# Performance work log

Hardware: AMD Instinct MI355X
Metric: run time of the kernel (lower is better)

The kernel has to match this reference:

```python
import jax, jax.numpy as jnp
import numpy as np

H = 16          # num_heads
LN_EPS = 1e-5   # torch LayerNorm default


def _ln(x, g, b):
    m = jnp.mean(x, axis=-1, keepdims=True)
    v = jnp.var(x, axis=-1, keepdims=True)
    return (x - m) * jax.lax.rsqrt(v + LN_EPS) * g + b


def _cross_attn(xq, xkv, wq, wk, wv, wp, bp):
    B, N, C = xq.shape
    d = C // H
    scale = d ** -0.5
    q = (xq @ wq).reshape(B, N, H, d).transpose(0, 2, 1, 3)   # bhnd
    k = (xkv @ wk).reshape(B, N, H, d).transpose(0, 2, 1, 3)
    v = (xkv @ wv).reshape(B, N, H, d).transpose(0, 2, 1, 3)
    attn = jax.nn.softmax(jnp.einsum('bhnd,bhmd->bhnm', q, k) * scale, axis=-1)
    out = jnp.einsum('bhnm,bhmd->bhnd', attn, v).transpose(0, 2, 1, 3).reshape(B, N, C)
    return out @ wp + bp


def setup_inputs() -> dict:
    key = jax.random.key(0)
    ks = jax.random.split(key, 16)
    B, N, C, Hid = 8, 1024, 1024, 4096
    s = 0.02
    inp = {
        'x_1': jax.random.normal(ks[0], (B, N, C), jnp.float32),
        'x_2': jax.random.normal(ks[1], (B, N, C), jnp.float32),
        'x_3': jax.random.normal(ks[2], (B, N, C), jnp.float32),
        'ln11_g': jnp.ones((C,), jnp.float32), 'ln11_b': jnp.zeros((C,), jnp.float32),
        'ln12_g': jnp.ones((C,), jnp.float32), 'ln12_b': jnp.zeros((C,), jnp.float32),
        'ln21_g': jnp.ones((C,), jnp.float32), 'ln21_b': jnp.zeros((C,), jnp.float32),
        'ln23_g': jnp.ones((C,), jnp.float32), 'ln23_b': jnp.zeros((C,), jnp.float32),
        'ln2_g': jnp.ones((C,), jnp.float32), 'ln2_b': jnp.zeros((C,), jnp.float32),
        'a1_wq': s * jax.random.normal(ks[3], (C, C), jnp.float32),
        'a1_wk': s * jax.random.normal(ks[4], (C, C), jnp.float32),
        'a1_wv': s * jax.random.normal(ks[5], (C, C), jnp.float32),
        'a1_wp': s * jax.random.normal(ks[6], (C, C), jnp.float32),
        'a1_bp': jnp.zeros((C,), jnp.float32),
        'a2_wq': s * jax.random.normal(ks[7], (C, C), jnp.float32),
        'a2_wk': s * jax.random.normal(ks[8], (C, C), jnp.float32),
        'a2_wv': s * jax.random.normal(ks[9], (C, C), jnp.float32),
        'a2_wp': s * jax.random.normal(ks[10], (C, C), jnp.float32),
        'a2_bp': jnp.zeros((C,), jnp.float32),
        'fc1_w': s * jax.random.normal(ks[11], (C, Hid), jnp.float32),
        'fc1_b': jnp.zeros((Hid,), jnp.float32),
        'fc2_w': s * jax.random.normal(ks[12], (Hid, C), jnp.float32),
        'fc2_b': jnp.zeros((C,), jnp.float32),
    }
    return inp


def reference(x_1, x_2, x_3,
              ln11_g, ln11_b, ln12_g, ln12_b, ln21_g, ln21_b, ln23_g, ln23_b,
              ln2_g, ln2_b,
              a1_wq, a1_wk, a1_wv, a1_wp, a1_bp,
              a2_wq, a2_wk, a2_wv, a2_wp, a2_bp,
              fc1_w, fc1_b, fc2_w, fc2_b):
    # dual cross-attention branches + residual (drop_path/dropout are identity at p=0)
    br1 = _cross_attn(_ln(x_1, ln11_g, ln11_b), _ln(x_2, ln12_g, ln12_b),
                      a1_wq, a1_wk, a1_wv, a1_wp, a1_bp)
    br2 = _cross_attn(_ln(x_1, ln21_g, ln21_b), _ln(x_3, ln23_g, ln23_b),
                      a2_wq, a2_wk, a2_wv, a2_wp, a2_bp)
    x = x_1 + br1 + br2
    # MLP block
    h = jax.nn.gelu(_ln(x, ln2_g, ln2_b) @ fc1_w + fc1_b, approximate=False)
    x = x + (h @ fc2_w + fc2_b)
    return x
```

## Files before the change

### kernel.cpp

```cpp
#include <hip/hip_runtime.h>
#include <hip/hip_bf16.h>
#include <cstdint>

typedef unsigned short u16;
typedef __bf16 v8bf __attribute__((ext_vector_type(8)));
typedef short v4s __attribute__((ext_vector_type(4)));
typedef float v4f __attribute__((ext_vector_type(4)));

__device__ __forceinline__ u16 f2bf(float f) {
  union { float f; uint32_t u; } v; v.f = f;
  return (u16)((v.u + 0x7fffu + ((v.u >> 16) & 1u)) >> 16);
}
__device__ __forceinline__ float bf2f(u16 u) {
  union { uint32_t u; float f; } v; v.u = ((uint32_t)u) << 16; return v.f;
}

#define GLL16(gsrc, ldst) \
  __builtin_amdgcn_global_load_lds((__attribute__((address_space(1))) void*)(gsrc), \
      (__attribute__((address_space(3))) void*)(ldst), 16, 0, 0)

#define TILE_MAP(blk, bm, bn) \
  int bm = ((blk) & 7) * 8 + (((blk) >> 3) & 7); \
  int bn = (blk) >> 6;

__device__ __forceinline__ void gemm_core(
    const u16* __restrict__ A, const u16* __restrict__ Bt, int K,
    char* la, char* lb, int bm, int bn, int tid, v4f acc[4][4])
{
  int wv = tid >> 6, lane = tid & 63, quad = lane >> 4, lc = lane & 15;
  int wm = wv & 1, wn = wv >> 1;
  for (int kt = 0; kt < K; kt += 64) {
    __syncthreads();
    #pragma unroll
    for (int c0 = 0; c0 < 4; ++c0) {
      int chunk = wv*4 + c0;
      int off = chunk*1024 + lane*16;
      int row = off >> 7;
      int sc  = (off >> 4) & 7;
      int lg  = sc ^ (row & 7);
      GLL16(A  + (size_t)(bm*128 + row) * K + kt + lg*8, la + chunk*1024);
      GLL16(Bt + (size_t)(bn*128 + row) * K + kt + lg*8, lb + chunk*1024);
    }
    __syncthreads();
    #pragma unroll
    for (int kc = 0; kc < 2; ++kc) {
      v8bf af[4], bfr[4];
      #pragma unroll
      for (int r = 0; r < 4; ++r) {
        int row = wm*64 + r*16 + lc;
        int sc = (kc*4 + quad) ^ (row & 7);
        af[r] = *(const v8bf*)(la + row*128 + sc*16);
      }
      #pragma unroll
      for (int c = 0; c < 4; ++c) {
        int row = wn*64 + c*16 + lc;
        int sc = (kc*4 + quad) ^ (row & 7);
        bfr[c] = *(const v8bf*)(lb + row*128 + sc*16);
      }
      #pragma unroll
      for (int r = 0; r < 4; ++r)
        #pragma unroll
        for (int c = 0; c < 4; ++c)
          acc[r][c] = __builtin_amdgcn_mfma_f32_16x16x32_bf16(af[r], bfr[c], acc[r][c], 0, 0, 0);
    }
  }
}

struct TDesc { const float* W; u16* WT; int K, N, tstart; };
struct PrepArgs {
  TDesc d[10];
  const float* lx[4]; const float* lg[4]; const float* lb_[4]; u16* lo[4];
  int ts;
};
__global__ __launch_bounds__(256) void prep_kernel(PrepArgs P)
{
  __shared__ float sh[32*33];
  int tid = threadIdx.x;
  if ((int)blockIdx.x < P.ts) {
    int bi = blockIdx.x;
    int idx = 0;
    #pragma unroll
    for (int i = 1; i < 10; ++i) if (bi >= P.d[i].tstart) idx = i;
    const float* W = P.d[idx].W;
    u16* WT = P.d[idx].WT;
    int K = P.d[idx].K, N = P.d[idx].N;
    int loc = bi - P.d[idx].tstart;
    int tiles_n = N >> 5;
    int bn = loc % tiles_n, bk = loc / tiles_n;
    int tx = tid & 31, ty = tid >> 5;
    #pragma unroll
    for (int j = 0; j < 4; ++j)
      sh[(ty + j*8)*33 + tx] = W[(size_t)(bk*32 + ty + j*8) * N + bn*32 + tx];
    __syncthreads();
    #pragma unroll
    for (int j = 0; j < 4; ++j)
      WT[(size_t)(bn*32 + ty + j*8) * K + bk*32 + tx] = f2bf(sh[tx*33 + ty + j*8]);
  } else {
    int lid = blockIdx.x - P.ts;
    int id = lid >> 13, row = lid & 8191;
    const float4* xr = (const float4*)(P.lx[id] + (size_t)row * 1024);
    float4 v = xr[tid];
    float s = v.x + v.y + v.z + v.w;
    float ss = v.x*v.x + v.y*v.y + v.z*v.z + v.w*v.w;
    for (int d = 1; d < 64; d <<= 1) { s += __shfl_xor(s, d); ss += __shfl_xor(ss, d); }
    int wv = tid >> 6, lane = tid & 63;
    if (lane == 0) { sh[wv] = s; sh[4 + wv] = ss; }
    __syncthreads();
    s  = sh[0] + sh[1] + sh[2] + sh[3];
    ss = sh[4] + sh[5] + sh[6] + sh[7];
    float mean = s * (1.f/1024.f);
    float var  = ss * (1.f/1024.f) - mean*mean;
    float rs = rsqrtf(var + 1e-5f);
    float4 gv = ((const float4*)P.lg[id])[tid];
    float4 bv = ((const float4*)P.lb_[id])[tid];
    ushort4 o;
    o.x = f2bf((v.x-mean)*rs*gv.x + bv.x);
    o.y = f2bf((v.y-mean)*rs*gv.y + bv.y);
    o.z = f2bf((v.z-mean)*rs*gv.z + bv.z);
    o.w = f2bf((v.w-mean)*rs*gv.w + bv.w);
    ((ushort4*)P.lo[id])[(size_t)row*256 + tid] = o;
  }
}

__global__ __launch_bounds__(256) void ln_bf16_kernel(
    const u16* __restrict__ x, const float* __restrict__ g, const float* __restrict__ bt,
    u16* __restrict__ out)
{
  int row = blockIdx.x, tid = threadIdx.x;
  ushort4 xr = ((const ushort4*)x)[(size_t)row*256 + tid];
  float4 v;
  v.x = bf2f(xr.x); v.y = bf2f(xr.y); v.z = bf2f(xr.z); v.w = bf2f(xr.w);
  float s = v.x + v.y + v.z + v.w;
  float ss = v.x*v.x + v.y*v.y + v.z*v.z + v.w*v.w;
  for (int d = 1; d < 64; d <<= 1) { s += __shfl_xor(s, d); ss += __shfl_xor(ss, d); }
  __shared__ float red[8];
  int wv = tid >> 6, lane = tid & 63;
  if (lane == 0) { red[wv] = s; red[4 + wv] = ss; }
  __syncthreads();
  s  = red[0] + red[1] + red[2] + red[3];
  ss = red[4] + red[5] + red[6] + red[7];
  float mean = s * (1.f/1024.f);
  float var  = ss * (1.f/1024.f) - mean*mean;
  float rs = rsqrtf(var + 1e-5f);
  float4 gv = ((const float4*)g)[tid];
  float4 bv = ((const float4*)bt)[tid];
  ushort4 o;
  o.x = f2bf((v.x-mean)*rs*gv.x + bv.x);
  o.y = f2bf((v.y-mean)*rs*gv.y + bv.y);
  o.z = f2bf((v.z-mean)*rs*gv.z + bv.z);
  o.w = f2bf((v.w-mean)*rs*gv.w + bv.w);
  ((ushort4*)out)[(size_t)row*256 + tid] = o;
}

struct QkvArgs { const u16* A[3]; const u16* Bt[3]; u16* C[3]; };
__global__ __launch_bounds__(256, 3) void gemm_qkv(QkvArgs P)
{
  int sub = blockIdx.x >> 9;
  int local = blockIdx.x & 511;
  TILE_MAP(local, bm, bn)
  int tid = threadIdx.x, wv = tid >> 6, lane = tid & 63, quad = lane >> 4, lc = lane & 15;
  int wm = wv & 1, wn = wv >> 1;
  __shared__ __align__(16) char lds_[32768];
  v4f acc[4][4] = {};
  gemm_core(P.A[sub], P.Bt[sub], 1024, lds_, lds_ + 16384, bm, bn, tid, acc);

  u16* Cout = P.C[sub];
  #pragma unroll
  for (int r = 0; r < 4; ++r) {
    int grow = bm*128 + wm*64 + r*16 + quad*4;
    #pragma unroll
    for (int c = 0; c < 4; ++c) {
      int gcol = bn*128 + wn*64 + c*16 + lc;
      if (sub == 2) {
        ushort4 o;
        o.x = f2bf(acc[r][c][0]); o.y = f2bf(acc[r][c][1]);
        o.z = f2bf(acc[r][c][2]); o.w = f2bf(acc[r][c][3]);
        *(ushort4*)(Cout + (size_t)gcol * 8192 + grow) = o;
      } else {
        #pragma unroll
        for (int i = 0; i < 4; ++i)
          Cout[(size_t)(grow + i) * 1024 + gcol] = f2bf(acc[r][c][i]);
      }
    }
  }
}

__device__ __forceinline__ void attn_body(
    const u16* __restrict__ Q, const u16* __restrict__ K, const u16* __restrict__ VT,
    u16* __restrict__ O, int bid, int tid, char* lds_)
{
  int qt = bid & 15, h = (bid >> 4) & 15, b = bid >> 8;
  int wv = tid >> 6, lane = tid & 63, quad = lane >> 4, lc = lane & 15;
  char* kt_l = lds_;
  char* vt_l = lds_ + 16384;
  const float scale = 0.125f;

  v8bf qf[2];
  {
    int qrow = qt*64 + wv*16 + lc;
    const u16* qp = Q + ((size_t)(b*1024 + qrow) * 1024 + h*64 + quad*8);
    qf[0] = *(const v8bf*)qp;
    qf[1] = *(const v8bf*)(qp + 32);
  }

  float m_i = -1e30f, l_i = 0.f;
  v4f oacc[4] = {};

  for (int it = 0; it < 8; ++it) {
    int kvb = it * 128;
    __syncthreads();
    #pragma unroll
    for (int c0 = 0; c0 < 4; ++c0) {
      int ch = wv*4 + c0;
      int off = ch*1024 + lane*16;
      {
        int row = off >> 7, sc = (off >> 4) & 7, lg = sc ^ (row & 7);
        GLL16(K + (size_t)(b*1024 + kvb + row) * 1024 + h*64 + lg*8, kt_l + ch*1024);
      }
      {
        int row = off >> 8, sc = (off >> 4) & 15, lg = sc ^ (row & 15);
        GLL16(VT + (size_t)(h*64 + row) * 8192 + b*1024 + kvb + lg*8, vt_l + ch*1024);
      }
    }
    __syncthreads();

    v4f s[8] = {};
    #pragma unroll
    for (int ct = 0; ct < 8; ++ct) {
      int row = ct*16 + lc;
      #pragma unroll
      for (int kc = 0; kc < 2; ++kc) {
        int sc = (kc*4 + quad) ^ (row & 7);
        v8bf kf = *(const v8bf*)(kt_l + row*128 + sc*16);
        s[ct] = __builtin_amdgcn_mfma_f32_16x16x32_bf16(kf, qf[kc], s[ct], 0, 0, 0);
      }
    }

    float mx = m_i;
    #pragma unroll
    for (int ct = 0; ct < 8; ++ct)
      #pragma unroll
      for (int i = 0; i < 4; ++i) mx = fmaxf(mx, s[ct][i] * scale);
    mx = fmaxf(mx, __shfl_xor(mx, 16));
    mx = fmaxf(mx, __shfl_xor(mx, 32));
    float alpha = __expf(m_i - mx);
    float rs = 0.f;
    #pragma unroll
    for (int ct = 0; ct < 8; ++ct)
      #pragma unroll
      for (int i = 0; i < 4; ++i) {
        float p = __expf(s[ct][i] * scale - mx);
        s[ct][i] = p;
        rs += p;
      }
    rs += __shfl_xor(rs, 16);
    rs += __shfl_xor(rs, 32);
    l_i = l_i * alpha + rs;
    m_i = mx;
    #pragma unroll
    for (int dt = 0; dt < 4; ++dt)
      #pragma unroll
      for (int i = 0; i < 4; ++i) oacc[dt][i] *= alpha;

    #pragma unroll
    for (int ct = 0; ct < 8; ++ct) {
      v4s pfrag;
      #pragma unroll
      for (int i = 0; i < 4; ++i) pfrag[i] = (short)f2bf(s[ct][i]);
      int lg = ct*2 + (quad >> 1);
      int ho = (quad & 1) * 8;
      #pragma unroll
      for (int dt = 0; dt < 4; ++dt) {
        int rowd = dt*16 + lc;
        int sc = lg ^ (rowd & 15);
        v4s vfrag = *(const v4s*)(vt_l + rowd*256 + sc*16 + ho);
        oacc[dt] = __builtin_amdgcn_mfma_f32_16x16x16bf16_1k(vfrag, pfrag, oacc[dt], 0, 0, 0);
      }
    }
  }

  __syncthreads();
  {
    char* base = kt_l + wv*2048;
    float inv = 1.f / l_i;
    #pragma unroll
    for (int dt = 0; dt < 4; ++dt) {
      ushort4 o;
      o.x = f2bf(oacc[dt][0]*inv); o.y = f2bf(oacc[dt][1]*inv);
      o.z = f2bf(oacc[dt][2]*inv); o.w = f2bf(oacc[dt][3]*inv);
      int lg = dt*2 + (quad >> 1);
      int sc = lg ^ (lc & 7);
      *(ushort4*)(base + lc*128 + sc*16 + (quad & 1)*8) = o;
    }
  }
  __syncthreads();
  {
    char* base = kt_l + wv*2048;
    #pragma unroll
    for (int rep = 0; rep < 2; ++rep) {
      int qr = rep*8 + (lane >> 3);
      int ch = lane & 7;
      int sc = ch ^ (qr & 7);
      uint4 d = *(const uint4*)(base + qr*128 + sc*16);
      *(uint4*)(O + (size_t)(b*1024 + qt*64 + wv*16 + qr) * 1024 + h*64 + ch*8) = d;
    }
  }
}

__global__ __launch_bounds__(256, 4) void attn_kernel(
    const u16* __restrict__ Q, const u16* __restrict__ K, const u16* __restrict__ VT,
    u16* __restrict__ O)
{
  __shared__ __align__(16) char lds_[32768];
  attn_body(Q, K, VT, O, blockIdx.x, threadIdx.x, lds_);
}

__global__ __launch_bounds__(256, 3) void attn_proj_kernel(
    const u16* __restrict__ Q, const u16* __restrict__ K, const u16* __restrict__ VT,
    u16* __restrict__ O,
    const u16* __restrict__ GA, const u16* __restrict__ GBt,
    const float* __restrict__ Gbias, u16* __restrict__ GC)
{
  __shared__ __align__(16) char lds_[32768];
  int tid = threadIdx.x;
  if ((int)blockIdx.x < 2048) {
    attn_body(Q, K, VT, O, blockIdx.x, tid, lds_);
  } else {
    int local = blockIdx.x - 2048;
    TILE_MAP(local, bm, bn)
    int wv = tid >> 6, lane = tid & 63, quad = lane >> 4, lc = lane & 15;
    int wm = wv & 1, wn = wv >> 1;
    v4f acc[4][4] = {};
    gemm_core(GA, GBt, 1024, lds_, lds_ + 16384, bm, bn, tid, acc);
    #pragma unroll
    for (int r = 0; r < 4; ++r) {
      int grow = bm*128 + wm*64 + r*16 + quad*4;
      #pragma unroll
      for (int c = 0; c < 4; ++c) {
        int gcol = bn*128 + wn*64 + c*16 + lc;
        float bv = Gbias[gcol];
        #pragma unroll
        for (int i = 0; i < 4; ++i)
          GC[(size_t)(grow + i) * 1024 + gcol] = f2bf(acc[r][c][i] + bv);
      }
    }
  }
}

__global__ __launch_bounds__(256, 3) void gemm_projadd(
    const u16* __restrict__ A, const u16* __restrict__ Bt,
    const float* __restrict__ bias, const float* __restrict__ x1,
    const u16* __restrict__ o1b, u16* __restrict__ xsum)
{
  TILE_MAP((int)blockIdx.x, bm, bn)
  int tid = threadIdx.x, wv = tid >> 6, lane = tid & 63, quad = lane >> 4, lc = lane & 15;
  int wm = wv & 1, wn = wv >> 1;
  __shared__ __align__(16) char lds_[32768];
  v4f acc[4][4] = {};
  gemm_core(A, Bt, 1024, lds_, lds_ + 16384, bm, bn, tid, acc);
  #pragma unroll
  for (int r = 0; r < 4; ++r) {
    int grow = bm*128 + wm*64 + r*16 + quad*4;
    #pragma unroll
    for (int c = 0; c < 4; ++c) {
      int gcol = bn*128 + wn*64 + c*16 + lc;
      float bv = bias[gcol];
      #pragma unroll
      for (int i = 0; i < 4; ++i) {
        size_t idx = (size_t)(grow + i) * 1024 + gcol;
        xsum[idx] = f2bf(acc[r][c][i] + bv + x1[idx] + bf2f(o1b[idx]));
      }
    }
  }
}

__global__ __launch_bounds__(256, 2) void gemm_fc1(
    const u16* __restrict__ A, const u16* __restrict__ Bt,
    const float* __restrict__ bias, u16* __restrict__ C)
{
  int bm = blockIdx.x >> 5, bn = blockIdx.x & 31;
  int tid = threadIdx.x, wv = tid >> 6, lane = tid & 63, quad = lane >> 4, lc = lane & 15;
  int wm = wv & 1, wn = wv >> 1;
  __shared__ __align__(16) char lds_[32768];
  v4f acc[4][4] = {};
  gemm_core(A, Bt, 1024, lds_, lds_ + 16384, bm, bn, tid, acc);
  #pragma unroll
  for (int r = 0; r < 4; ++r) {
    int grow = bm*128 + wm*64 + r*16 + quad*4;
    #pragma unroll
    for (int c = 0; c < 4; ++c) {
      int gcol = bn*128 + wn*64 + c*16 + lc;
      float bv = bias[gcol];
      #pragma unroll
      for (int i = 0; i < 4; ++i) {
        float v = acc[r][c][i] + bv;
        float u2 = fminf(1.5957691216f * (v + 0.044715f * v * v * v), 80.f);
        float t = __expf(u2);
        float ge = v * t / (t + 1.f);
        C[(size_t)(grow + i) * 4096 + gcol] = f2bf(ge);
      }
    }
  }
}

__global__ __launch_bounds__(256, 3) void gemm_fc2(
    const u16* __restrict__ A, const u16* __restrict__ Bt,
    const float* __restrict__ bias, const u16* __restrict__ r1,
    float* __restrict__ C)
{
  TILE_MAP((int)blockIdx.x, bm, bn)
  int tid = threadIdx.x, wv = tid >> 6, lane = tid & 63, quad = lane >> 4, lc = lane & 15;
  int wm = wv & 1, wn = wv >> 1;
  __shared__ __align__(16) char lds_[32768];
  v4f acc[4][4] = {};
  gemm_core(A, Bt, 4096, lds_, lds_ + 16384, bm, bn, tid, acc);
  #pragma unroll
  for (int r = 0; r < 4; ++r) {
    int grow = bm*128 + wm*64 + r*16 + quad*4;
    #pragma unroll
    for (int c = 0; c < 4; ++c) {
      int gcol = bn*128 + wn*64 + c*16 + lc;
      float bv = bias[gcol];
      #pragma unroll
      for (int i = 0; i < 4; ++i) {
        size_t idx = (size_t)(grow + i) * 1024 + gcol;
        C[idx] = acc[r][c][i] + bv + bf2f(r1[idx]);
      }
    }
  }
}

extern "C" void kernel_launch(void* const* d_in, const int* in_sizes, int n_in,
                              void* d_out, int out_size, void* d_ws, size_t ws_size,
                              hipStream_t stream)
{
  const float* x1    = (const float*)d_in[0];
  const float* x2    = (const float*)d_in[1];
  const float* x3    = (const float*)d_in[2];
  const float* ln11g = (const float*)d_in[3];
  const float* ln11b = (const float*)d_in[4];
  const float* ln12g = (const float*)d_in[5];
  const float* ln12b = (const float*)d_in[6];
  const float* ln21g = (const float*)d_in[7];
  const float* ln21b = (const float*)d_in[8];
  const float* ln23g = (const float*)d_in[9];
  const float* ln23b = (const float*)d_in[10];
  const float* ln2g  = (const float*)d_in[11];
  const float* ln2b  = (const float*)d_in[12];
  const float* a1wq  = (const float*)d_in[13];
  const float* a1wk  = (const float*)d_in[14];
  const float* a1wv  = (const float*)d_in[15];
  const float* a1wp  = (const float*)d_in[16];
  const float* a1bp  = (const float*)d_in[17];
  const float* a2wq  = (const float*)d_in[18];
  const float* a2wk  = (const float*)d_in[19];
  const float* a2wv  = (const float*)d_in[20];
  const float* a2wp  = (const float*)d_in[21];
  const float* a2bp  = (const float*)d_in[22];
  const float* fc1w  = (const float*)d_in[23];
  const float* fc1b  = (const float*)d_in[24];
  const float* fc2w  = (const float*)d_in[25];
  const float* fc2b  = (const float*)d_in[26];

  char* ws = (char*)d_ws;
  const size_t MB = (size_t)1 << 20;
  u16* wtq1 = (u16*)(ws + 0*MB);  u16* wtk1 = (u16*)(ws + 2*MB);
  u16* wtv1 = (u16*)(ws + 4*MB);  u16* wtp1 = (u16*)(ws + 6*MB);
  u16* wtq2 = (u16*)(ws + 8*MB);  u16* wtk2 = (u16*)(ws + 10*MB);
  u16* wtv2 = (u16*)(ws + 12*MB); u16* wtp2 = (u16*)(ws + 14*MB);
  u16* wtf1 = (u16*)(ws + 16*MB); u16* wtf2 = (u16*)(ws + 24*MB);
  u16* xq1  = (u16*)(ws + 32*MB); u16* xkv1 = (u16*)(ws + 48*MB);
  u16* xq2  = (u16*)(ws + 64*MB); u16* xkv2 = (u16*)(ws + 80*MB);
  u16* Qb   = (u16*)(ws + 96*MB); u16* Kb   = (u16*)(ws + 112*MB);
  u16* VTb  = (u16*)(ws + 128*MB);
  u16* O1   = (u16*)(ws + 32*MB);
  u16* O2   = (u16*)(ws + 48*MB);
  u16* o1b  = (u16*)(ws + 64*MB);
  u16* xsum = (u16*)(ws + 112*MB);
  u16* ln2o = (u16*)(ws + 32*MB);
  u16* hbuf = (u16*)(ws + 48*MB);

  dim3 blk(256);

  PrepArgs pa;
  const float* Ws[10]  = {a1wq, a1wk, a1wv, a1wp, a2wq, a2wk, a2wv, a2wp, fc1w, fc2w};
  u16* WTs[10]         = {wtq1, wtk1, wtv1, wtp1, wtq2, wtk2, wtv2, wtp2, wtf1, wtf2};
  int Kd[10] = {1024,1024,1024,1024,1024,1024,1024,1024,1024,4096};
  int Nd[10] = {1024,1024,1024,1024,1024,1024,1024,1024,4096,1024};
  int ts = 0;
  for (int i = 0; i < 10; ++i) {
    pa.d[i] = {Ws[i], WTs[i], Kd[i], Nd[i], ts};
    ts += (Kd[i]/32) * (Nd[i]/32);
  }
  pa.ts = ts;
  pa.lx[0]=x1; pa.lg[0]=ln11g; pa.lb_[0]=ln11b; pa.lo[0]=xq1;
  pa.lx[1]=x2; pa.lg[1]=ln12g; pa.lb_[1]=ln12b; pa.lo[1]=xkv1;
  pa.lx[2]=x1; pa.lg[2]=ln21g; pa.lb_[2]=ln21b; pa.lo[2]=xq2;
  pa.lx[3]=x3; pa.lg[3]=ln23g; pa.lb_[3]=ln23b; pa.lo[3]=xkv2;
  prep_kernel<<<ts + 32768, blk, 0, stream>>>(pa);

  QkvArgs g1;
  g1.A[0]=xq1;  g1.Bt[0]=wtq1; g1.C[0]=Qb;
  g1.A[1]=xkv1; g1.Bt[1]=wtk1; g1.C[1]=Kb;
  g1.A[2]=xkv1; g1.Bt[2]=wtv1; g1.C[2]=VTb;
  gemm_qkv<<<1536, blk, 0, stream>>>(g1);

  attn_kernel<<<2048, blk, 0, stream>>>(Qb, Kb, VTb, O1);

  QkvArgs g2;
  g2.A[0]=xq2;  g2.Bt[0]=wtq2; g2.C[0]=Qb;
  g2.A[1]=xkv2; g2.Bt[1]=wtk2; g2.C[1]=Kb;
  g2.A[2]=xkv2; g2.Bt[2]=wtv2; g2.C[2]=VTb;
  gemm_qkv<<<1536, blk, 0, stream>>>(g2);

  attn_proj_kernel<<<2048 + 512, blk, 0, stream>>>(Qb, Kb, VTb, O2, O1, wtp1, a1bp, o1b);

  gemm_projadd<<<512, blk, 0, stream>>>(O2, wtp2, a2bp, x1, o1b, xsum);

  ln_bf16_kernel<<<8192, blk, 0, stream>>>(xsum, ln2g, ln2b, ln2o);

  gemm_fc1<<<2048, blk, 0, stream>>>(ln2o, wtf1, fc1b, hbuf);

  gemm_fc2<<<512, blk, 0, stream>>>(hbuf, wtf2, fc2b, xsum, (float*)d_out);
}
```

Measured before the change: 664.3 us.

## Use 256x256 eight-wave pipelined GEMM core for QKV and FC1

Adds a new GEMM core that uses 256x256 output tiles with 512 threads (8 waves) and a double-buffered 128KB LDS. Global-to-LDS loads are staggered across quarter-phases with explicit barriers, waitcnt and setprio around the MFMA groups. The QKV and FC1 kernels switch to this core, which quadruples data reuse per block and overlaps loads with compute. In exchange it uses more registers and LDS, gets fewer blocks per CU, and launches fewer blocks per grid, which may hurt load balance across the CUs.

```diff
diff --git a/kernel.cpp b/kernel.cpp
--- a/kernel.cpp
+++ b/kernel.cpp
@@ -64,6 +64,106 @@
           acc[r][c] = __builtin_amdgcn_mfma_f32_16x16x32_bf16(af[r], bfr[c], acc[r][c], 0, 0, 0);
     }
   }
+}
+
+template<int NT>
+__device__ __forceinline__ void gemm8_core(
+    const u16* __restrict__ A, const u16* __restrict__ Bt,
+    char* lds, int bm, int bn, int tid, v4f acc[8][4])
+{
+  constexpr int K = NT * 64;
+  int wid = tid >> 6, lane = tid & 63, quad = lane >> 4, lc = lane & 15;
+  int wm = wid >> 2, wn = wid & 3;
+
+  int ch0 = wid*2, ch1 = wid*2 + 1;
+  int r0 = ch0*8 + (lane >> 3), r1 = ch1*8 + (lane >> 3);
+  int lg0 = (lane & 7) ^ (r0 & 7), lg1 = (lane & 7) ^ (r1 & 7);
+  const u16* gA0 = A  + (size_t)(bm*256 + r0) * K + lg0*8;
+  const u16* gA1 = A  + (size_t)(bm*256 + r1) * K + lg1*8;
+  const u16* gB0 = Bt + (size_t)(bn*256 + r0) * K + lg0*8;
+  const u16* gB1 = Bt + (size_t)(bn*256 + r1) * K + lg1*8;
+  int dA0 = ch0*1024, dA1 = ch1*1024;
+
+  auto STAGE_A = [&](int h, int tile, int buf) {
+    GLL16(gA0 + (size_t)h*128*K + tile*64, lds + buf*32768 + h*16384 + dA0);
+    GLL16(gA1 + (size_t)h*128*K + tile*64, lds + buf*32768 + h*16384 + dA1);
+  };
+  auto STAGE_B = [&](int h, int tile, int buf) {
+    GLL16(gB0 + (size_t)h*128*K + tile*64, lds + 65536 + buf*32768 + h*16384 + dA0);
+    GLL16(gB1 + (size_t)h*128*K + tile*64, lds + 65536 + buf*32768 + h*16384 + dA1);
+  };
+
+  int s0 = quad ^ (lc & 7);
+  const char* rA0 = lds + ((wm*128 + lc)*128 + s0*16);
+  const char* rA1 = lds + ((wm*128 + lc)*128 + (s0^4)*16);
+  const char* rB0 = lds + 65536 + ((wn*64 + lc)*128 + s0*16);
+  const char* rB1 = lds + 65536 + ((wn*64 + lc)*128 + (s0^4)*16);
+
+  v8bf a[4][2], b0[2][2], b1[2][2];
+
+#define RD_A(qm) do { _Pragma("unroll") for (int mf = 0; mf < 4; ++mf) { \
+    a[mf][0] = *(const v8bf*)(rA0 + bsel*32768 + (qm)*8192 + mf*2048); \
+    a[mf][1] = *(const v8bf*)(rA1 + bsel*32768 + (qm)*8192 + mf*2048); } } while(0)
+#define RD_B(qn, bb) do { _Pragma("unroll") for (int nf = 0; nf < 2; ++nf) { \
+    bb[nf][0] = *(const v8bf*)(rB0 + bsel*32768 + (qn)*4096 + nf*2048); \
+    bb[nf][1] = *(const v8bf*)(rB1 + bsel*32768 + (qn)*4096 + nf*2048); } } while(0)
+#define MFMAQ(qm, bb, qn) do { \
+    __builtin_amdgcn_s_setprio(1); \
+    _Pragma("unroll") for (int mf = 0; mf < 4; ++mf) \
+    _Pragma("unroll") for (int nf = 0; nf < 2; ++nf) \
+    _Pragma("unroll") for (int kc = 0; kc < 2; ++kc) \
+      acc[(qm)*4+mf][(qn)*2+nf] = __builtin_amdgcn_mfma_f32_16x16x32_bf16( \
+          a[mf][kc], bb[nf][kc], acc[(qm)*4+mf][(qn)*2+nf], 0, 0, 0); \
+    __builtin_amdgcn_s_setprio(0); } while(0)
+#define LGKM0 do { asm volatile("s_waitcnt lgkmcnt(0)" ::: "memory"); \
+    __builtin_amdgcn_sched_barrier(0); } while(0)
+
+#define GROUP(t, bs) do { \
+    const int bsel = (bs); const int nsel = bsel ^ 1; \
+     \
+    RD_A(0); RD_B(0, b0); \
+    if ((t)+1 < NT) STAGE_A(0, (t)+1, nsel); \
+    __builtin_amdgcn_s_barrier(); LGKM0; \
+    MFMAQ(0, b0, 0); \
+    __builtin_amdgcn_s_barrier(); \
+     \
+    RD_B(1, b1); \
+    if ((t)+1 < NT) STAGE_A(1, (t)+1, nsel); \
+    __builtin_amdgcn_s_barrier(); LGKM0; \
+    MFMAQ(0, b1, 1); \
+    __builtin_amdgcn_s_barrier(); \
+     \
+    RD_A(1); \
+    if ((t)+2 < NT) STAGE_B(0, (t)+2, bsel); \
+    __builtin_amdgcn_s_barrier(); LGKM0; \
+    MFMAQ(1, b1, 1); \
+    __builtin_amdgcn_s_barrier(); \
+     \
+    if ((t)+2 < NT) STAGE_B(1, (t)+2, bsel); \
+    __builtin_amdgcn_s_barrier(); \
+    MFMAQ(1, b0, 0); \
+    if ((t) < NT-2)       asm volatile("s_waitcnt vmcnt(4)" ::: "memory"); \
+    else if ((t) == NT-2) asm volatile("s_waitcnt vmcnt(0)" ::: "memory"); \
+    __builtin_amdgcn_s_barrier(); \
+  } while(0)
+
+  STAGE_B(0, 0, 0); STAGE_B(1, 0, 0);
+  STAGE_A(0, 0, 0); STAGE_A(1, 0, 0);
+  STAGE_B(0, 1, 1); STAGE_B(1, 1, 1);
+  asm volatile("s_waitcnt vmcnt(4)" ::: "memory");
+  __builtin_amdgcn_s_barrier();
+
+  #pragma unroll 1
+  for (int ti = 0; ti < NT; ti += 2) {
+    GROUP(ti, 0);
+    GROUP(ti + 1, 1);
+  }
+
+#undef RD_A
+#undef RD_B
+#undef MFMAQ
+#undef LGKM0
+#undef GROUP
 }
 
 struct TDesc { const float* W; u16* WT; int K, N, tstart; };
@@ -153,33 +253,33 @@
 }
 
 struct QkvArgs { const u16* A[3]; const u16* Bt[3]; u16* C[3]; };
-__global__ __launch_bounds__(256, 3) void gemm_qkv(QkvArgs P)
-{
-  int sub = blockIdx.x >> 9;
-  int local = blockIdx.x & 511;
-  TILE_MAP(local, bm, bn)
-  int tid = threadIdx.x, wv = tid >> 6, lane = tid & 63, quad = lane >> 4, lc = lane & 15;
-  int wm = wv & 1, wn = wv >> 1;
-  __shared__ __align__(16) char lds_[32768];
-  v4f acc[4][4] = {};
-  gemm_core(P.A[sub], P.Bt[sub], 1024, lds_, lds_ + 16384, bm, bn, tid, acc);
-
+__global__ __launch_bounds__(512, 2) void gemm8_qkv(QkvArgs P)
+{
+  __shared__ __align__(16) char lds8[131072];
+  int sub = blockIdx.x >> 7;
+  int local = blockIdx.x & 127;
+  int bm = (local & 7)*4 + ((local >> 3) & 3), bn = local >> 5;
+  v4f acc[8][4] = {};
+  gemm8_core<16>(P.A[sub], P.Bt[sub], lds8, bm, bn, threadIdx.x, acc);
+
+  int tid = threadIdx.x, wid = tid >> 6, lane = tid & 63, quad = lane >> 4, lc = lane & 15;
+  int wm = wid >> 2, wn = wid & 3;
   u16* Cout = P.C[sub];
   #pragma unroll
-  for (int r = 0; r < 4; ++r) {
-    int grow = bm*128 + wm*64 + r*16 + quad*4;
-    #pragma unroll
-    for (int c = 0; c < 4; ++c) {
-      int gcol = bn*128 + wn*64 + c*16 + lc;
+  for (int mf = 0; mf < 8; ++mf) {
+    int grow = bm*256 + wm*128 + mf*16 + quad*4;
+    #pragma unroll
+    for (int nf = 0; nf < 4; ++nf) {
+      int gcol = bn*256 + wn*64 + nf*16 + lc;
       if (sub == 2) {
         ushort4 o;
-        o.x = f2bf(acc[r][c][0]); o.y = f2bf(acc[r][c][1]);
-        o.z = f2bf(acc[r][c][2]); o.w = f2bf(acc[r][c][3]);
+        o.x = f2bf(acc[mf][nf][0]); o.y = f2bf(acc[mf][nf][1]);
+        o.z = f2bf(acc[mf][nf][2]); o.w = f2bf(acc[mf][nf][3]);
         *(ushort4*)(Cout + (size_t)gcol * 8192 + grow) = o;
       } else {
         #pragma unroll
         for (int i = 0; i < 4; ++i)
-          Cout[(size_t)(grow + i) * 1024 + gcol] = f2bf(acc[r][c][i]);
+          Cout[(size_t)(grow + i) * 1024 + gcol] = f2bf(acc[mf][nf][i]);
       }
     }
   }
@@ -374,26 +474,28 @@
   }
 }
 
-__global__ __launch_bounds__(256, 2) void gemm_fc1(
+__global__ __launch_bounds__(512, 2) void gemm_fc1(
     const u16* __restrict__ A, const u16* __restrict__ Bt,
     const float* __restrict__ bias, u16* __restrict__ C)
 {
-  int bm = blockIdx.x >> 5, bn = blockIdx.x & 31;
-  int tid = threadIdx.x, wv = tid >> 6, lane = tid & 63, quad = lane >> 4, lc = lane & 15;
-  int wm = wv & 1, wn = wv >> 1;
-  __shared__ __align__(16) char lds_[32768];
-  v4f acc[4][4] = {};
-  gemm_core(A, Bt, 1024, lds_, lds_ + 16384, bm, bn, tid, acc);
+  __shared__ __align__(16) char lds8[131072];
+  int blk = blockIdx.x;
+  int bm = (blk & 7)*4 + ((blk >> 3) & 3), bn = blk >> 5;
+  v4f acc[8][4] = {};
+  gemm8_core<16>(A, Bt, lds8, bm, bn, threadIdx.x, acc);
+
+  int tid = threadIdx.x, wid = tid >> 6, lane = tid & 63, quad = lane >> 4, lc = lane & 15;
+  int wm = wid >> 2, wn = wid & 3;
   #pragma unroll
-  for (int r = 0; r < 4; ++r) {
-    int grow = bm*128 + wm*64 + r*16 + quad*4;
-    #pragma unroll
-    for (int c = 0; c < 4; ++c) {
-      int gcol = bn*128 + wn*64 + c*16 + lc;
-      float bv = bias[gcol];
+  for (int nf = 0; nf < 4; ++nf) {
+    int gcol = bn*256 + wn*64 + nf*16 + lc;
+    float bv = bias[gcol];
+    #pragma unroll
+    for (int mf = 0; mf < 8; ++mf) {
+      int grow = bm*256 + wm*128 + mf*16 + quad*4;
       #pragma unroll
       for (int i = 0; i < 4; ++i) {
-        float v = acc[r][c][i] + bv;
+        float v = acc[mf][nf][i] + bv;
         float u2 = fminf(1.5957691216f * (v + 0.044715f * v * v * v), 80.f);
         float t = __expf(u2);
         float ge = v * t / (t + 1.f);
@@ -481,6 +583,7 @@
   u16* hbuf = (u16*)(ws + 48*MB);
 
   dim3 blk(256);
+  dim3 blk8(512);
 
   PrepArgs pa;
   const float* Ws[10]  = {a1wq, a1wk, a1wv, a1wp, a2wq, a2wk, a2wv, a2wp, fc1w, fc2w};
@@ -503,7 +606,7 @@
   g1.A[0]=xq1;  g1.Bt[0]=wtq1; g1.C[0]=Qb;
   g1.A[1]=xkv1; g1.Bt[1]=wtk1; g1.C[1]=Kb;
   g1.A[2]=xkv1; g1.Bt[2]=wtv1; g1.C[2]=VTb;
-  gemm_qkv<<<1536, blk, 0, stream>>>(g1);
+  gemm8_qkv<<<384, blk8, 0, stream>>>(g1);
 
   attn_kernel<<<2048, blk, 0, stream>>>(Qb, Kb, VTb, O1);
 
@@ -511,7 +614,7 @@
   g2.A[0]=xq2;  g2.Bt[0]=wtq2; g2.C[0]=Qb;
   g2.A[1]=xkv2; g2.Bt[1]=wtk2; g2.C[1]=Kb;
   g2.A[2]=xkv2; g2.Bt[2]=wtv2; g2.C[2]=VTb;
-  gemm_qkv<<<1536, blk, 0, stream>>>(g2);
+  gemm8_qkv<<<384, blk8, 0, stream>>>(g2);
 
   attn_proj_kernel<<<2048 + 512, blk, 0, stream>>>(Qb, Kb, VTb, O2, O1, wtp1, a1bp, o1b);
 
@@ -519,7 +622,7 @@
 
   ln_bf16_kernel<<<8192, blk, 0, stream>>>(xsum, ln2g, ln2b, ln2o);
 
-  gemm_fc1<<<2048, blk, 0, stream>>>(ln2o, wtf1, fc1b, hbuf);
+  gemm_fc1<<<512, blk8, 0, stream>>>(ln2o, wtf1, fc1b, hbuf);
 
   gemm_fc2<<<512, blk, 0, stream>>>(hbuf, wtf2, fc2b, xsum, (float*)d_out);
 }
```

After: 709.1 us. +6.7%, slower.

## Split prep, overlap late weight prep with QKV GEMM, stage epilogues through LDS

Applied to the files above, without the earlier changes.

The monolithic prep kernel is split. Only the weights and LayerNorms needed by the first QKV GEMM run up front, and the x1 LayerNorm pair is fused so x1 is read once. The remaining weight transposes and the x3 LayerNorm are appended as extra blocks to the first QKV GEMM launch so they fill the machine alongside it. GEMM epilogues now write bf16 tiles into swizzled LDS and sweep them out as coalesced 16-byte row stores, replacing scattered 2-byte global writes. Softmax and GELU switch to the raw v_exp_f32 base-2 instruction with prescaled constants, which adds register pressure and extra syncs in the epilogues.

```diff
diff --git a/kernel.cpp b/kernel.cpp
--- a/kernel.cpp
+++ b/kernel.cpp
@@ -13,6 +13,9 @@
 }
 __device__ __forceinline__ float bf2f(u16 u) {
   union { uint32_t u; float f; } v; v.u = ((uint32_t)u) << 16; return v.f;
+}
+__device__ __forceinline__ float ex2(float x) {
+  float r; asm("v_exp_f32 %0, %1" : "=v"(r) : "v"(x)); return r;
 }
 
 #define GLL16(gsrc, ldst) \
@@ -66,59 +69,121 @@
   }
 }
 
+__device__ __forceinline__ void lds_put16(char* lds_, int row, int col, u16 v) {
+  *(u16*)(lds_ + row*256 + (((col >> 4) ^ (row & 7)) << 5) + (col & 15)*2) = v;
+}
+__device__ __forceinline__ void sweep128(const char* lds_, u16* gout, size_t ldc, int tid) {
+  int sub = tid >> 4, j = tid & 15;
+  #pragma unroll
+  for (int p = 0; p < 8; ++p) {
+    int row = p*16 + sub;
+    uint4 d = *(const uint4*)(lds_ + row*256 + ((((j >> 1) ^ (row & 7)) << 5) + ((j & 1) << 4)));
+    *(uint4*)(gout + (size_t)row*ldc + j*8) = d;
+  }
+}
+
 struct TDesc { const float* W; u16* WT; int K, N, tstart; };
-struct PrepArgs {
-  TDesc d[10];
-  const float* lx[4]; const float* lg[4]; const float* lb_[4]; u16* lo[4];
-  int ts;
+
+__device__ __forceinline__ void do_transpose(const TDesc& D, int loc, int tid, float* sh) {
+  const float* W = D.W;
+  u16* WT = D.WT;
+  int K = D.K, N = D.N;
+  int tiles_n = N >> 5;
+  int bn = loc % tiles_n, bk = loc / tiles_n;
+  int tx = tid & 31, ty = tid >> 5;
+  #pragma unroll
+  for (int j = 0; j < 4; ++j)
+    sh[(ty + j*8)*33 + tx] = W[(size_t)(bk*32 + ty + j*8) * N + bn*32 + tx];
+  __syncthreads();
+  #pragma unroll
+  for (int j = 0; j < 4; ++j)
+    WT[(size_t)(bn*32 + ty + j*8) * K + bk*32 + tx] = f2bf(sh[tx*33 + ty + j*8]);
+}
+
+__device__ __forceinline__ void ln_f32_row(const float* x, const float* g, const float* b,
+                                           u16* out, int row, int tid, float* red)
+{
+  float4 v = ((const float4*)(x + (size_t)row * 1024))[tid];
+  float s = v.x + v.y + v.z + v.w;
+  float ss = v.x*v.x + v.y*v.y + v.z*v.z + v.w*v.w;
+  for (int d = 1; d < 64; d <<= 1) { s += __shfl_xor(s, d); ss += __shfl_xor(ss, d); }
+  int wv = tid >> 6, lane = tid & 63;
+  if (lane == 0) { red[wv] = s; red[4 + wv] = ss; }
+  __syncthreads();
+  s  = red[0] + red[1] + red[2] + red[3];
+  ss = red[4] + red[5] + red[6] + red[7];
+  float mean = s * (1.f/1024.f);
+  float var  = ss * (1.f/1024.f) - mean*mean;
+  float rs = rsqrtf(var + 1e-5f);
+  float4 gv = ((const float4*)g)[tid];
+  float4 bv = ((const float4*)b)[tid];
+  ushort4 o;
+  o.x = f2bf((v.x-mean)*rs*gv.x + bv.x);
+  o.y = f2bf((v.y-mean)*rs*gv.y + bv.y);
+  o.z = f2bf((v.z-mean)*rs*gv.z + bv.z);
+  o.w = f2bf((v.w-mean)*rs*gv.w + bv.w);
+  ((ushort4*)out)[(size_t)row*256 + tid] = o;
+}
+
+__device__ __forceinline__ void ln_f32_row2(const float* x,
+    const float* g1, const float* b1, const float* g2, const float* b2,
+    u16* o1, u16* o2, int row, int tid, float* red)
+{
+  float4 v = ((const float4*)(x + (size_t)row * 1024))[tid];
+  float s = v.x + v.y + v.z + v.w;
+  float ss = v.x*v.x + v.y*v.y + v.z*v.z + v.w*v.w;
+  for (int d = 1; d < 64; d <<= 1) { s += __shfl_xor(s, d); ss += __shfl_xor(ss, d); }
+  int wv = tid >> 6, lane = tid & 63;
+  if (lane == 0) { red[wv] = s; red[4 + wv] = ss; }
+  __syncthreads();
+  s  = red[0] + red[1] + red[2] + red[3];
+  ss = red[4] + red[5] + red[6] + red[7];
+  float mean = s * (1.f/1024.f);
+  float var  = ss * (1.f/1024.f) - mean*mean;
+  float rs = rsqrtf(var + 1e-5f);
+  float4 xn;
+  xn.x = (v.x-mean)*rs; xn.y = (v.y-mean)*rs; xn.z = (v.z-mean)*rs; xn.w = (v.w-mean)*rs;
+  {
+    float4 gv = ((const float4*)g1)[tid];
+    float4 bv = ((const float4*)b1)[tid];
+    ushort4 o;
+    o.x = f2bf(xn.x*gv.x + bv.x); o.y = f2bf(xn.y*gv.y + bv.y);
+    o.z = f2bf(xn.z*gv.z + bv.z); o.w = f2bf(xn.w*gv.w + bv.w);
+    ((ushort4*)o1)[(size_t)row*256 + tid] = o;
+  }
+  {
+    float4 gv = ((const float4*)g2)[tid];
+    float4 bv = ((const float4*)b2)[tid];
+    ushort4 o;
+    o.x = f2bf(xn.x*gv.x + bv.x); o.y = f2bf(xn.y*gv.y + bv.y);
+    o.z = f2bf(xn.z*gv.z + bv.z); o.w = f2bf(xn.w*gv.w + bv.w);
+    ((ushort4*)o2)[(size_t)row*256 + tid] = o;
+  }
+}
+
+struct PrepA {
+  TDesc d[3];
+  const float *x1, *g11, *b11, *g21, *b21;
+  const float *x2, *g12, *b12;
+  u16 *xq1, *xq2, *xkv1;
+  int tsa;
 };
-__global__ __launch_bounds__(256) void prep_kernel(PrepArgs P)
+__global__ __launch_bounds__(256) void prep_a_kernel(PrepA P)
 {
   __shared__ float sh[32*33];
   int tid = threadIdx.x;
-  if ((int)blockIdx.x < P.ts) {
-    int bi = blockIdx.x;
+  int bi = blockIdx.x;
+  if (bi < P.tsa) {
     int idx = 0;
     #pragma unroll
-    for (int i = 1; i < 10; ++i) if (bi >= P.d[i].tstart) idx = i;
-    const float* W = P.d[idx].W;
-    u16* WT = P.d[idx].WT;
-    int K = P.d[idx].K, N = P.d[idx].N;
-    int loc = bi - P.d[idx].tstart;
-    int tiles_n = N >> 5;
-    int bn = loc % tiles_n, bk = loc / tiles_n;
-    int tx = tid & 31, ty = tid >> 5;
-    #pragma unroll
-    for (int j = 0; j < 4; ++j)
-      sh[(ty + j*8)*33 + tx] = W[(size_t)(bk*32 + ty + j*8) * N + bn*32 + tx];
-    __syncthreads();
-    #pragma unroll
-    for (int j = 0; j < 4; ++j)
-      WT[(size_t)(bn*32 + ty + j*8) * K + bk*32 + tx] = f2bf(sh[tx*33 + ty + j*8]);
+    for (int i = 1; i < 3; ++i) if (bi >= P.d[i].tstart) idx = i;
+    do_transpose(P.d[idx], bi - P.d[idx].tstart, tid, sh);
   } else {
-    int lid = blockIdx.x - P.ts;
-    int id = lid >> 13, row = lid & 8191;
-    const float4* xr = (const float4*)(P.lx[id] + (size_t)row * 1024);
-    float4 v = xr[tid];
-    float s = v.x + v.y + v.z + v.w;
-    float ss = v.x*v.x + v.y*v.y + v.z*v.z + v.w*v.w;
-    for (int d = 1; d < 64; d <<= 1) { s += __shfl_xor(s, d); ss += __shfl_xor(ss, d); }
-    int wv = tid >> 6, lane = tid & 63;
-    if (lane == 0) { sh[wv] = s; sh[4 + wv] = ss; }
-    __syncthreads();
-    s  = sh[0] + sh[1] + sh[2] + sh[3];
-    ss = sh[4] + sh[5] + sh[6] + sh[7];
-    float mean = s * (1.f/1024.f);
-    float var  = ss * (1.f/1024.f) - mean*mean;
-    float rs = rsqrtf(var + 1e-5f);
-    float4 gv = ((const float4*)P.lg[id])[tid];
-    float4 bv = ((const float4*)P.lb_[id])[tid];
-    ushort4 o;
-    o.x = f2bf((v.x-mean)*rs*gv.x + bv.x);
-    o.y = f2bf((v.y-mean)*rs*gv.y + bv.y);
-    o.z = f2bf((v.z-mean)*rs*gv.z + bv.z);
-    o.w = f2bf((v.w-mean)*rs*gv.w + bv.w);
-    ((ushort4*)P.lo[id])[(size_t)row*256 + tid] = o;
+    int lid = bi - P.tsa;
+    if (lid < 8192)
+      ln_f32_row2(P.x1, P.g11, P.b11, P.g21, P.b21, P.xq1, P.xq2, lid, tid, sh);
+    else
+      ln_f32_row(P.x2, P.g12, P.b12, P.xkv1, lid - 8192, tid, sh);
   }
 }
 
@@ -153,34 +218,77 @@
 }
 
 struct QkvArgs { const u16* A[3]; const u16* Bt[3]; u16* C[3]; };
-__global__ __launch_bounds__(256, 3) void gemm_qkv(QkvArgs P)
-{
-  int sub = blockIdx.x >> 9;
-  int local = blockIdx.x & 511;
+
+__device__ __forceinline__ void qkv_body(const QkvArgs& P, int blk, int tid, char* lds_)
+{
+  int sub = blk >> 9;
+  int local = blk & 511;
   TILE_MAP(local, bm, bn)
-  int tid = threadIdx.x, wv = tid >> 6, lane = tid & 63, quad = lane >> 4, lc = lane & 15;
+  int wv = tid >> 6, lane = tid & 63, quad = lane >> 4, lc = lane & 15;
   int wm = wv & 1, wn = wv >> 1;
-  __shared__ __align__(16) char lds_[32768];
   v4f acc[4][4] = {};
   gemm_core(P.A[sub], P.Bt[sub], 1024, lds_, lds_ + 16384, bm, bn, tid, acc);
-
   u16* Cout = P.C[sub];
-  #pragma unroll
-  for (int r = 0; r < 4; ++r) {
-    int grow = bm*128 + wm*64 + r*16 + quad*4;
-    #pragma unroll
-    for (int c = 0; c < 4; ++c) {
-      int gcol = bn*128 + wn*64 + c*16 + lc;
-      if (sub == 2) {
-        ushort4 o;
-        o.x = f2bf(acc[r][c][0]); o.y = f2bf(acc[r][c][1]);
-        o.z = f2bf(acc[r][c][2]); o.w = f2bf(acc[r][c][3]);
-        *(ushort4*)(Cout + (size_t)gcol * 8192 + grow) = o;
-      } else {
+  __syncthreads();
+  if (sub == 2) {
+    #pragma unroll
+    for (int r = 0; r < 4; ++r) {
+      int rl = wm*64 + r*16 + quad*4;
+      #pragma unroll
+      for (int c = 0; c < 4; ++c) {
+        int cl = wn*64 + c*16 + lc;
         #pragma unroll
         for (int i = 0; i < 4; ++i)
-          Cout[(size_t)(grow + i) * 1024 + gcol] = f2bf(acc[r][c][i]);
-      }
+          lds_put16(lds_, cl, rl + i, f2bf(acc[r][c][i]));
+      }
+    }
+    __syncthreads();
+    sweep128(lds_, Cout + (size_t)(bn*128) * 8192 + bm*128, 8192, tid);
+  } else {
+    #pragma unroll
+    for (int r = 0; r < 4; ++r) {
+      int lrow = wm*64 + r*16 + quad*4;
+      #pragma unroll
+      for (int c = 0; c < 4; ++c) {
+        int lcol = wn*64 + c*16 + lc;
+        #pragma unroll
+        for (int i = 0; i < 4; ++i)
+          lds_put16(lds_, lrow + i, lcol, f2bf(acc[r][c][i]));
+      }
+    }
+    __syncthreads();
+    sweep128(lds_, Cout + (size_t)(bm*128) * 1024 + bn*128, 1024, tid);
+  }
+}
+
+__global__ __launch_bounds__(256, 3) void gemm_qkv(QkvArgs P)
+{
+  __shared__ __align__(16) char lds_[32768];
+  qkv_body(P, blockIdx.x, threadIdx.x, lds_);
+}
+
+struct PrepB {
+  TDesc d[7];
+  const float *x3, *g23, *b23;
+  u16 *xkv2;
+  int tsb;
+};
+__global__ __launch_bounds__(256, 3) void qkv_prep_kernel(QkvArgs P, PrepB Q)
+{
+  __shared__ __align__(16) char lds_[32768];
+  int tid = threadIdx.x;
+  if ((int)blockIdx.x < 1536) {
+    qkv_body(P, blockIdx.x, tid, lds_);
+  } else {
+    float* sh = (float*)lds_;
+    int bi = blockIdx.x - 1536;
+    if (bi < Q.tsb) {
+      int idx = 0;
+      #pragma unroll
+      for (int i = 1; i < 7; ++i) if (bi >= Q.d[i].tstart) idx = i;
+      do_transpose(Q.d[idx], bi - Q.d[idx].tstart, tid, sh);
+    } else {
+      ln_f32_row(Q.x3, Q.g23, Q.b23, Q.xkv2, bi - Q.tsb, tid, sh);
     }
   }
 }
@@ -193,7 +301,7 @@
   int wv = tid >> 6, lane = tid & 63, quad = lane >> 4, lc = lane & 15;
   char* kt_l = lds_;
   char* vt_l = lds_ + 16384;
-  const float scale = 0.125f;
+  const float cl2 = 0.18033688f;
 
   v8bf qf[2];
   {
@@ -236,20 +344,24 @@
       }
     }
 
+    #pragma unroll
+    for (int ct = 0; ct < 8; ++ct)
+      #pragma unroll
+      for (int i = 0; i < 4; ++i) s[ct][i] *= cl2;
     float mx = m_i;
     #pragma unroll
     for (int ct = 0; ct < 8; ++ct)
       #pragma unroll
-      for (int i = 0; i < 4; ++i) mx = fmaxf(mx, s[ct][i] * scale);
+      for (int i = 0; i < 4; ++i) mx = fmaxf(mx, s[ct][i]);
     mx = fmaxf(mx, __shfl_xor(mx, 16));
     mx = fmaxf(mx, __shfl_xor(mx, 32));
-    float alpha = __expf(m_i - mx);
+    float alpha = ex2(m_i - mx);
     float rs = 0.f;
     #pragma unroll
     for (int ct = 0; ct < 8; ++ct)
       #pragma unroll
       for (int i = 0; i < 4; ++i) {
-        float p = __expf(s[ct][i] * scale - mx);
+        float p = ex2(s[ct][i] - mx);
         s[ct][i] = p;
         rs += p;
       }
@@ -332,18 +444,21 @@
     int wm = wv & 1, wn = wv >> 1;
     v4f acc[4][4] = {};
     gemm_core(GA, GBt, 1024, lds_, lds_ + 16384, bm, bn, tid, acc);
+    __syncthreads();
     #pragma unroll
     for (int r = 0; r < 4; ++r) {
-      int grow = bm*128 + wm*64 + r*16 + quad*4;
+      int lrow = wm*64 + r*16 + quad*4;
       #pragma unroll
       for (int c = 0; c < 4; ++c) {
-        int gcol = bn*128 + wn*64 + c*16 + lc;
-        float bv = Gbias[gcol];
+        int lcol = wn*64 + c*16 + lc;
+        float bv = Gbias[bn*128 + lcol];
         #pragma unroll
         for (int i = 0; i < 4; ++i)
-          GC[(size_t)(grow + i) * 1024 + gcol] = f2bf(acc[r][c][i] + bv);
-      }
-    }
+          lds_put16(lds_, lrow + i, lcol, f2bf(acc[r][c][i] + bv));
+      }
+    }
+    __syncthreads();
+    sweep128(lds_, GC + (size_t)(bm*128) * 1024 + bn*128, 1024, tid);
   }
 }
 
@@ -358,20 +473,25 @@
   __shared__ __align__(16) char lds_[32768];
   v4f acc[4][4] = {};
   gemm_core(A, Bt, 1024, lds_, lds_ + 16384, bm, bn, tid, acc);
+  __syncthreads();
   #pragma unroll
   for (int r = 0; r < 4; ++r) {
-    int grow = bm*128 + wm*64 + r*16 + quad*4;
+    int lrow = wm*64 + r*16 + quad*4;
+    int grow = bm*128 + lrow;
     #pragma unroll
     for (int c = 0; c < 4; ++c) {
-      int gcol = bn*128 + wn*64 + c*16 + lc;
+      int lcol = wn*64 + c*16 + lc;
+      int gcol = bn*128 + lcol;
       float bv = bias[gcol];
       #pragma unroll
       for (int i = 0; i < 4; ++i) {
         size_t idx = (size_t)(grow + i) * 1024 + gcol;
-        xsum[idx] = f2bf(acc[r][c][i] + bv + x1[idx] + bf2f(o1b[idx]));
-      }
-    }
-  }
+        lds_put16(lds_, lrow + i, lcol, f2bf(acc[r][c][i] + bv + x1[idx] + bf2f(o1b[idx])));
+      }
+    }
+  }
+  __syncthreads();
+  sweep128(lds_, xsum + (size_t)(bm*128) * 1024 + bn*128, 1024, tid);
 }
 
 __global__ __launch_bounds__(256, 2) void gemm_fc1(
@@ -384,23 +504,25 @@
   __shared__ __align__(16) char lds_[32768];
   v4f acc[4][4] = {};
   gemm_core(A, Bt, 1024, lds_, lds_ + 16384, bm, bn, tid, acc);
+  __syncthreads();
   #pragma unroll
   for (int r = 0; r < 4; ++r) {
-    int grow = bm*128 + wm*64 + r*16 + quad*4;
+    int lrow = wm*64 + r*16 + quad*4;
     #pragma unroll
     for (int c = 0; c < 4; ++c) {
-      int gcol = bn*128 + wn*64 + c*16 + lc;
-      float bv = bias[gcol];
+      int lcol = wn*64 + c*16 + lc;
+      float bv = bias[bn*128 + lcol];
       #pragma unroll
       for (int i = 0; i < 4; ++i) {
         float v = acc[r][c][i] + bv;
-        float u2 = fminf(1.5957691216f * (v + 0.044715f * v * v * v), 80.f);
-        float t = __expf(u2);
-        float ge = v * t / (t + 1.f);
-        C[(size_t)(grow + i) * 4096 + gcol] = f2bf(ge);
-      }
-    }
-  }
+        float u2 = fminf(2.3023840f * (v + 0.044715f * v * v * v), 115.f);
+        float t = ex2(u2);
+        lds_put16(lds_, lrow + i, lcol, f2bf(v * t / (t + 1.f)));
+      }
+    }
+  }
+  __syncthreads();
+  sweep128(lds_, C + (size_t)(bm*128) * 4096 + bn*128, 4096, tid);
 }
 
 __global__ __launch_bounds__(256, 3) void gemm_fc2(
@@ -482,28 +604,38 @@
 
   dim3 blk(256);
 
-  PrepArgs pa;
-  const float* Ws[10]  = {a1wq, a1wk, a1wv, a1wp, a2wq, a2wk, a2wv, a2wp, fc1w, fc2w};
-  u16* WTs[10]         = {wtq1, wtk1, wtv1, wtp1, wtq2, wtk2, wtv2, wtp2, wtf1, wtf2};
-  int Kd[10] = {1024,1024,1024,1024,1024,1024,1024,1024,1024,4096};
-  int Nd[10] = {1024,1024,1024,1024,1024,1024,1024,1024,4096,1024};
-  int ts = 0;
-  for (int i = 0; i < 10; ++i) {
-    pa.d[i] = {Ws[i], WTs[i], Kd[i], Nd[i], ts};
-    ts += (Kd[i]/32) * (Nd[i]/32);
-  }
-  pa.ts = ts;
-  pa.lx[0]=x1; pa.lg[0]=ln11g; pa.lb_[0]=ln11b; pa.lo[0]=xq1;
-  pa.lx[1]=x2; pa.lg[1]=ln12g; pa.lb_[1]=ln12b; pa.lo[1]=xkv1;
-  pa.lx[2]=x1; pa.lg[2]=ln21g; pa.lb_[2]=ln21b; pa.lo[2]=xq2;
-  pa.lx[3]=x3; pa.lg[3]=ln23g; pa.lb_[3]=ln23b; pa.lo[3]=xkv2;
-  prep_kernel<<<ts + 32768, blk, 0, stream>>>(pa);
+  PrepA pa;
+  {
+    const float* Ws[3] = {a1wq, a1wk, a1wv};
+    u16* WTs[3]        = {wtq1, wtk1, wtv1};
+    int ts = 0;
+    for (int i = 0; i < 3; ++i) { pa.d[i] = {Ws[i], WTs[i], 1024, 1024, ts}; ts += 1024; }
+    pa.tsa = ts;
+  }
+  pa.x1 = x1; pa.g11 = ln11g; pa.b11 = ln11b; pa.g21 = ln21g; pa.b21 = ln21b;
+  pa.x2 = x2; pa.g12 = ln12g; pa.b12 = ln12b;
+  pa.xq1 = xq1; pa.xq2 = xq2; pa.xkv1 = xkv1;
+  prep_a_kernel<<<pa.tsa + 16384, blk, 0, stream>>>(pa);
 
   QkvArgs g1;
   g1.A[0]=xq1;  g1.Bt[0]=wtq1; g1.C[0]=Qb;
   g1.A[1]=xkv1; g1.Bt[1]=wtk1; g1.C[1]=Kb;
   g1.A[2]=xkv1; g1.Bt[2]=wtv1; g1.C[2]=VTb;
-  gemm_qkv<<<1536, blk, 0, stream>>>(g1);
+  PrepB pb;
+  {
+    const float* Ws[7] = {a1wp, a2wq, a2wk, a2wv, a2wp, fc1w, fc2w};
+    u16* WTs[7]        = {wtp1, wtq2, wtk2, wtv2, wtp2, wtf1, wtf2};
+    int Kd[7] = {1024,1024,1024,1024,1024,1024,4096};
+    int Nd[7] = {1024,1024,1024,1024,1024,4096,1024};
+    int ts = 0;
+    for (int i = 0; i < 7; ++i) {
+      pb.d[i] = {Ws[i], WTs[i], Kd[i], Nd[i], ts};
+      ts += (Kd[i]/32) * (Nd[i]/32);
+    }
+    pb.tsb = ts;
+  }
+  pb.x3 = x3; pb.g23 = ln23g; pb.b23 = ln23b; pb.xkv2 = xkv2;
+  qkv_prep_kernel<<<1536 + pb.tsb + 8192, blk, 0, stream>>>(g1, pb);
 
   attn_kernel<<<2048, blk, 0, stream>>>(Qb, Kb, VTb, O1);
 
```

After: 693.5 us. 1.04x slower.
